# Kernel tuning notes

Hardware: AMD Instinct MI355X
Metric: run time of the kernel (lower is better)

## Reference

```python
import jax, jax.numpy as jnp
import numpy as np

TOP_K = 2
NUM_EXPERTS = 16
CAPACITY = 512          # >> avg load (128/expert) so no token is ever dropped in practice
FP8_MAX = 448.0         # float8_e4m3fn max representable magnitude


def _fp8_quant(v, axes):
    """Simulated fp8 e4m3 dynamic quantization: amax scaling + clipping.
    Returns (quantized values, scale with keepdims)."""
    s = jnp.clip(jnp.max(jnp.abs(v), axis=axes, keepdims=True) / FP8_MAX, 1e-12, None)
    return jnp.clip(v / s, -FP8_MAX, FP8_MAX), s


def setup_inputs() -> dict:
    key = jax.random.key(0)
    k0, k1, k2, k3 = jax.random.split(key, 4)
    T, H, I, E = 1024, 2048, 1408, NUM_EXPERTS
    x = jax.random.normal(k0, (T, H), jnp.float32)
    router_logits = jax.random.normal(k1, (T, E), jnp.float32)
    w13_weight = jax.random.normal(k2, (E, 2 * I, H), jnp.float32) * 0.02
    w2_weight = jax.random.normal(k3, (E, H, I), jnp.float32) * 0.02
    return {"x": x, "router_logits": router_logits,
            "w13_weight": w13_weight, "w2_weight": w2_weight}


def reference(x, router_logits, w13_weight, w2_weight):
    T, H = x.shape
    E, K, C = NUM_EXPERTS, TOP_K, CAPACITY
    I = w2_weight.shape[2]

    # --- routing: softmax -> top-k -> renormalize ---
    probs = jax.nn.softmax(router_logits, axis=-1)               # [T, E]
    topw, topi = jax.lax.top_k(probs, K)                          # [T, K]
    topw = topw / jnp.sum(topw, axis=-1, keepdims=True)

    # --- dispatch: flatten (token, k) rows, rank within expert ---
    rid = topi.reshape(-1)                                        # [T*K] expert id per row
    rtok = jnp.arange(T * K) // K                                 # source token per row
    order = jnp.argsort(rid)                                      # jax sort is stable
    counts = jnp.bincount(rid, length=E)
    offsets = jnp.concatenate([jnp.zeros(1, counts.dtype), jnp.cumsum(counts)[:-1]])
    pos_sorted = jnp.arange(T * K) - offsets[rid[order]]
    pos = jnp.zeros(T * K, jnp.int32).at[order].set(pos_sorted.astype(jnp.int32))
    valid = pos < C                                               # capacity is generous: no drops
    posc = jnp.minimum(pos, C - 1)

    xrows = x[rtok] * valid[:, None].astype(x.dtype)              # [T*K, H]
    xbuf = jnp.zeros((E, C, H), x.dtype).at[rid, posc].add(xrows)  # [E, C, H]

    # --- grouped GEMM 1 (gate+up), fp8 w8a8: per-expert weight scale, per-token act scale ---
    w13q, sw13 = _fp8_quant(w13_weight, (1, 2))                   # sw13 [E,1,1]
    xq, sa1 = _fp8_quant(xbuf, -1)                                # sa1  [E,C,1]
    h = jnp.einsum('ech,efh->ecf', xq, w13q) * (sa1 * sw13)       # [E, C, 2I]

    # --- silu_and_mul ---
    gate, up = h[..., :I], h[..., I:]
    act = jax.nn.silu(gate) * up                                  # [E, C, I]

    # --- grouped GEMM 2 (down) ---
    w2q, sw2 = _fp8_quant(w2_weight, (1, 2))                      # sw2 [E,1,1]
    aq, sa2 = _fp8_quant(act, -1)                                 # sa2 [E,C,1]
    ybuf = jnp.einsum('eci,ehi->ech', aq, w2q) * (sa2 * sw2)      # [E, C, H]

    # --- combine: gather back and weight by router probs ---
    yrows = ybuf[rid, posc] * valid[:, None].astype(x.dtype)      # [T*K, H]
    out = jnp.einsum('tkh,tk->th', yrows.reshape(T, K, H), topw)  # [T, H]
    return out
```

## Files before the change

kernel.cpp:

```cpp
#include <hip/hip_runtime.h>
#include <hip/hip_bf16.h>
#include <math.h>

#define NEXP 16
#define CAP  512
#define TTOK 1024
#define HDIM 2048
#define IDIM 1408

typedef float fx4 __attribute__((ext_vector_type(4)));
typedef short short8 __attribute__((ext_vector_type(8)));
typedef unsigned int u32;
typedef unsigned long long u64;

__device__ __forceinline__ unsigned short f2bf(float f) {
    u32 u = __float_as_uint(f);
    u += 0x7FFFu + ((u >> 16) & 1u);
    return (unsigned short)(u >> 16);
}
__device__ __forceinline__ float bf2f(unsigned short h) {
    return __uint_as_float(((u32)h) << 16);
}

__global__ void router_kernel(const float* __restrict__ logits,
                              int* __restrict__ topi, float* __restrict__ topw,
                              int* __restrict__ cnt1) {
    int t = blockIdx.x * blockDim.x + threadIdx.x;
    if (t >= TTOK) return;
    const float* l = logits + t * NEXP;
    float b0 = -INFINITY, b1 = -INFINITY; int i0 = 0, i1 = 0;
    for (int e = 0; e < NEXP; ++e) {
        float v = l[e];
        if (v > b0) { b1 = b0; i1 = i0; b0 = v; i0 = e; }
        else if (v > b1) { b1 = v; i1 = e; }
    }
    float w0 = 1.f / (1.f + expf(b1 - b0));
    topi[t*2]   = i0; topi[t*2+1] = i1;
    topw[t*2]   = w0; topw[t*2+1] = 1.f - w0;
    atomicAdd(&cnt1[i0], 1);
    atomicAdd(&cnt1[i1], 1);
}

__global__ void scan_kernel(const int* __restrict__ cnt1, int* __restrict__ base) {
    if (threadIdx.x == 0 && blockIdx.x == 0) {
        int s = 0;
        for (int e = 0; e < NEXP; ++e) {
            base[e] = s;
            int c = cnt1[e]; if (c > CAP) c = CAP;
            s += c;
        }
        base[NEXP] = s;
    }
}

__global__ void assign_kernel(const int* __restrict__ topi, const int* __restrict__ base,
                              int* __restrict__ cnt2,
                              int* __restrict__ slot_token, int* __restrict__ slot_of) {
    int t = blockIdx.x * blockDim.x + threadIdx.x;
    if (t >= TTOK) return;
    for (int k = 0; k < 2; ++k) {
        int e = topi[t*2+k];
        int p = atomicAdd(&cnt2[e], 1);
        if (p < CAP) {
            int s = base[e] + p;
            slot_token[s] = t;
            slot_of[t*2+k] = s;
        } else {
            slot_of[t*2+k] = -1;
        }
    }
}

#define LDA 40

template<int NDIM, int KDIM, bool GATHER>
__global__ __launch_bounds__(256) void gemm_bt_kernel(
    const float* __restrict__ Af32,
    const unsigned short* __restrict__ Abf16,
    const float* __restrict__ W,
    unsigned short* __restrict__ Cout,
    const int* __restrict__ slot_token,
    const int* __restrict__ base)
{
    const int e = blockIdx.z;
    const int n0 = base[e];
    const int rows = base[e+1] - n0;
    const int rtile = blockIdx.y * 128;
    if (rtile >= rows) return;
    const int col0 = blockIdx.x * 128;

    __shared__ unsigned short sA[128 * LDA];
    __shared__ unsigned short sB[128 * LDA];

    const int tid = threadIdx.x;
    const int lane = tid & 63;
    const int wv = tid >> 6;
    const int wm = wv >> 1, wn = wv & 1;
    const int lr = lane & 15;
    const int quad = lane >> 4;

    fx4 acc[4][4];
    #pragma unroll
    for (int i = 0; i < 4; ++i)
        #pragma unroll
        for (int j = 0; j < 4; ++j) acc[i][j] = (fx4)0.f;

    int tok[4];
    if (GATHER) {
        int rr = tid >> 3;
        #pragma unroll
        for (int p = 0; p < 4; ++p) {
            int grow = rtile + rr + p*32;
            tok[p] = (grow < rows) ? slot_token[n0 + grow] : -1;
        }
    } else {
        int rr = tid >> 2;
        #pragma unroll
        for (int p = 0; p < 2; ++p) {
            int grow = rtile + rr + p*64;
            tok[p] = (grow < rows) ? (n0 + grow) : -1;
        }
    }

    const float* Wp = W + ((size_t)e * NDIM + col0) * KDIM;

    const int KT = KDIM / 32;
    for (int kt = 0; kt < KT; ++kt) {
        const int k0 = kt * 32;
        __syncthreads();
        if (GATHER) {
            int g = tid & 7, rr = tid >> 3;
            #pragma unroll
            for (int p = 0; p < 4; ++p) {
                int row = rr + p*32;
                u64 v = 0;
                if (tok[p] >= 0) {
                    fx4 f = *(const fx4*)(Af32 + (size_t)tok[p]*KDIM + k0 + g*4);
                    u32 lo = (u32)f2bf(f.x) | ((u32)f2bf(f.y) << 16);
                    u32 hi = (u32)f2bf(f.z) | ((u32)f2bf(f.w) << 16);
                    v = (u64)lo | ((u64)hi << 32);
                }
                *(u64*)&sA[row*LDA + g*4] = v;
            }
        } else {
            int g = tid & 3, rr = tid >> 2;
            #pragma unroll
            for (int p = 0; p < 2; ++p) {
                int row = rr + p*64;
                fx4 v = (fx4)0.f;
                if (tok[p] >= 0)
                    v = *(const fx4*)(Abf16 + (size_t)tok[p]*KDIM + k0 + g*8);
                *(fx4*)&sA[row*LDA + g*8] = v;
            }
        }
        {
            int g = tid & 7, rr = tid >> 3;
            #pragma unroll
            for (int p = 0; p < 4; ++p) {
                int row = rr + p*32;
                fx4 f = *(const fx4*)(Wp + (size_t)row*KDIM + k0 + g*4);
                u32 lo = (u32)f2bf(f.x) | ((u32)f2bf(f.y) << 16);
                u32 hi = (u32)f2bf(f.z) | ((u32)f2bf(f.w) << 16);
                *(u64*)&sB[row*LDA + g*4] = (u64)lo | ((u64)hi << 32);
            }
        }
        __syncthreads();
        short8 af[4], bfr[4];
        #pragma unroll
        for (int mi = 0; mi < 4; ++mi) {
            int row = wm*64 + mi*16 + lr;
            af[mi] = *(const short8*)&sA[row*LDA + quad*8];
        }
        #pragma unroll
        for (int ni = 0; ni < 4; ++ni) {
            int row = wn*64 + ni*16 + lr;
            bfr[ni] = *(const short8*)&sB[row*LDA + quad*8];
        }
        #pragma unroll
        for (int mi = 0; mi < 4; ++mi)
            #pragma unroll
            for (int ni = 0; ni < 4; ++ni)
                acc[mi][ni] = __builtin_amdgcn_mfma_f32_16x16x32_bf16(
                    af[mi], bfr[ni], acc[mi][ni], 0, 0, 0);
    }

    #pragma unroll
    for (int mi = 0; mi < 4; ++mi) {
        #pragma unroll
        for (int r = 0; r < 4; ++r) {
            int grow = rtile + wm*64 + mi*16 + quad*4 + r;
            if (grow < rows) {
                size_t orow = (size_t)(n0 + grow) * NDIM;
                #pragma unroll
                for (int ni = 0; ni < 4; ++ni) {
                    int gcol = col0 + wn*64 + ni*16 + lr;
                    Cout[orow + gcol] = f2bf(acc[mi][ni][r]);
                }
            }
        }
    }
}

__global__ void silu_kernel(const unsigned short* __restrict__ h,
                            unsigned short* __restrict__ act,
                            const int* __restrict__ base) {
    const int R = base[NEXP];
    int idx = blockIdx.x * blockDim.x + threadIdx.x;
    int row = idx / (IDIM/8);
    int j   = idx % (IDIM/8);
    if (row >= R) return;
    const unsigned short* g = h + (size_t)row * (2*IDIM) + j*8;
    const unsigned short* u = g + IDIM;
    unsigned short go[8], uo[8], ao[8];
    *(fx4*)go = *(const fx4*)g;
    *(fx4*)uo = *(const fx4*)u;
    #pragma unroll
    for (int i = 0; i < 8; ++i) {
        float gv = bf2f(go[i]), uv = bf2f(uo[i]);
        float s = gv / (1.f + __expf(-gv));
        ao[i] = f2bf(s * uv);
    }
    *(fx4*)&act[(size_t)row*IDIM + j*8] = *(fx4*)ao;
}

__global__ void combine_kernel(const unsigned short* __restrict__ ybuf,
                               const int* __restrict__ slot_of,
                               const float* __restrict__ topw,
                               float* __restrict__ out) {
    int t = blockIdx.x;
    int c = threadIdx.x * 8;
    int s0 = slot_of[t*2], s1 = slot_of[t*2+1];
    float w0 = topw[t*2], w1 = topw[t*2+1];
    float res[8];
    #pragma unroll
    for (int i = 0; i < 8; ++i) res[i] = 0.f;
    if (s0 >= 0) {
        unsigned short y[8];
        *(fx4*)y = *(const fx4*)(ybuf + (size_t)s0*HDIM + c);
        #pragma unroll
        for (int i = 0; i < 8; ++i) res[i] += w0 * bf2f(y[i]);
    }
    if (s1 >= 0) {
        unsigned short y[8];
        *(fx4*)y = *(const fx4*)(ybuf + (size_t)s1*HDIM + c);
        #pragma unroll
        for (int i = 0; i < 8; ++i) res[i] += w1 * bf2f(y[i]);
    }
    float* o = out + (size_t)t*HDIM + c;
    *(fx4*)o       = *(fx4*)res;
    *(fx4*)(o + 4) = *(fx4*)(res + 4);
}

extern "C" void kernel_launch(void* const* d_in, const int* in_sizes, int n_in,
                              void* d_out, int out_size, void* d_ws, size_t ws_size,
                              hipStream_t stream) {
    const float* x      = (const float*)d_in[0];
    const float* logits = (const float*)d_in[1];
    const float* w13    = (const float*)d_in[2];
    const float* w2     = (const float*)d_in[3];
    float* out = (float*)d_out;

    char* ws = (char*)d_ws;
    size_t off = 0;
    auto alloc = [&](size_t bytes) -> void* {
        void* p = ws + off;
        off += (bytes + 255) & ~(size_t)255;
        return p;
    };
    int*   topi       = (int*)  alloc(TTOK*2*sizeof(int));
    float* topw       = (float*)alloc(TTOK*2*sizeof(float));
    int*   cnt1       = (int*)  alloc(NEXP*sizeof(int));
    int*   cnt2       = (int*)  alloc(NEXP*sizeof(int));
    int*   base       = (int*)  alloc((NEXP+1)*sizeof(int));
    int*   slot_token = (int*)  alloc(TTOK*2*sizeof(int));
    int*   slot_of    = (int*)  alloc(TTOK*2*sizeof(int));
    unsigned short* h    = (unsigned short*)alloc((size_t)TTOK*2 * (2*IDIM) * 2);
    unsigned short* act  = (unsigned short*)alloc((size_t)TTOK*2 * IDIM * 2);
    unsigned short* ybuf = (unsigned short*)alloc((size_t)TTOK*2 * HDIM * 2);

    hipMemsetAsync(cnt1, 0, NEXP*sizeof(int), stream);
    hipMemsetAsync(cnt2, 0, NEXP*sizeof(int), stream);

    router_kernel<<<dim3((TTOK+255)/256), 256, 0, stream>>>(logits, topi, topw, cnt1);
    scan_kernel<<<1, 64, 0, stream>>>(cnt1, base);
    assign_kernel<<<dim3((TTOK+255)/256), 256, 0, stream>>>(topi, base, cnt2, slot_token, slot_of);

    gemm_bt_kernel<2*IDIM, HDIM, true>
        <<<dim3(2*IDIM/128, CAP/128, NEXP), 256, 0, stream>>>(
            x, nullptr, w13, h, slot_token, base);

    silu_kernel<<<dim3((TTOK*2*(IDIM/8) + 255)/256), 256, 0, stream>>>(h, act, base);

    gemm_bt_kernel<HDIM, IDIM, false>
        <<<dim3(HDIM/128, CAP/128, NEXP), 256, 0, stream>>>(
            nullptr, act, w2, ybuf, slot_token, base);

    combine_kernel<<<dim3(TTOK), 256, 0, stream>>>(ybuf, slot_of, topw, out);
}
```

Before: 784.2 us.

## Double-buffer GEMM tiles with register prefetch and narrow N tile to 64

The grouped GEMM kernel now keeps two LDS buffers and loads the next K-slice's global data into registers while MFMAs run on the current slice, so there is one barrier per iteration instead of two. The output tile shrinks from 128x128 to 128x64, with each wave covering 32 rows by 64 columns, which doubles the grid along N. The goal is to hide global memory latency and raise the block count to fill the device. In exchange, A-tile loads and fp32-to-bf16 conversions are repeated across twice as many column blocks, and MFMA work per LDS load drops.

```diff
diff --git a/kernel.cpp b/kernel.cpp
--- a/kernel.cpp
+++ b/kernel.cpp
@@ -20,6 +20,11 @@
 }
 __device__ __forceinline__ float bf2f(unsigned short h) {
     return __uint_as_float(((u32)h) << 16);
+}
+__device__ __forceinline__ u64 pack4bf(fx4 f) {
+    u32 lo = (u32)f2bf(f.x) | ((u32)f2bf(f.y) << 16);
+    u32 hi = (u32)f2bf(f.z) | ((u32)f2bf(f.w) << 16);
+    return (u64)lo | ((u64)hi << 32);
 }
 
 __global__ void router_kernel(const float* __restrict__ logits,
@@ -87,113 +92,118 @@
     const int rows = base[e+1] - n0;
     const int rtile = blockIdx.y * 128;
     if (rtile >= rows) return;
-    const int col0 = blockIdx.x * 128;
-
-    __shared__ unsigned short sA[128 * LDA];
-    __shared__ unsigned short sB[128 * LDA];
+    const int col0 = blockIdx.x * 64;
+
+    __shared__ unsigned short sA[2][128 * LDA];
+    __shared__ unsigned short sB[2][64 * LDA];
 
     const int tid = threadIdx.x;
     const int lane = tid & 63;
     const int wv = tid >> 6;
-    const int wm = wv >> 1, wn = wv & 1;
     const int lr = lane & 15;
     const int quad = lane >> 4;
 
-    fx4 acc[4][4];
+    fx4 acc[2][4];
     #pragma unroll
-    for (int i = 0; i < 4; ++i)
+    for (int i = 0; i < 2; ++i)
         #pragma unroll
         for (int j = 0; j < 4; ++j) acc[i][j] = (fx4)0.f;
+
+    const int bg = tid & 7, bc = tid >> 3;
+    const int ag = tid & 7, ar = tid >> 3;
+    const int ag2 = tid & 3, ar2 = tid >> 2;
 
     int tok[4];
     if (GATHER) {
-        int rr = tid >> 3;
         #pragma unroll
         for (int p = 0; p < 4; ++p) {
-            int grow = rtile + rr + p*32;
+            int grow = rtile + ar + p*32;
             tok[p] = (grow < rows) ? slot_token[n0 + grow] : -1;
         }
     } else {
-        int rr = tid >> 2;
         #pragma unroll
         for (int p = 0; p < 2; ++p) {
-            int grow = rtile + rr + p*64;
+            int grow = rtile + ar2 + p*64;
             tok[p] = (grow < rows) ? (n0 + grow) : -1;
         }
     }
 
     const float* Wp = W + ((size_t)e * NDIM + col0) * KDIM;
+
+    fx4 pa[4], pb[2];
+
+    auto prefetch = [&](int k0) {
+        #pragma unroll
+        for (int p = 0; p < 2; ++p)
+            pb[p] = *(const fx4*)(Wp + (size_t)(bc + p*32) * KDIM + k0 + bg*4);
+        if (GATHER) {
+            #pragma unroll
+            for (int p = 0; p < 4; ++p)
+                pa[p] = (tok[p] >= 0)
+                    ? *(const fx4*)(Af32 + (size_t)tok[p]*KDIM + k0 + ag*4)
+                    : (fx4)0.f;
+        } else {
+            #pragma unroll
+            for (int p = 0; p < 2; ++p)
+                pa[p] = (tok[p] >= 0)
+                    ? *(const fx4*)(Abf16 + (size_t)tok[p]*KDIM + k0 + ag2*8)
+                    : (fx4)0.f;
+        }
+    };
+    auto stage = [&](int buf) {
+        #pragma unroll
+        for (int p = 0; p < 2; ++p)
+            *(u64*)&sB[buf][(bc + p*32)*LDA + bg*4] = pack4bf(pb[p]);
+        if (GATHER) {
+            #pragma unroll
+            for (int p = 0; p < 4; ++p)
+                *(u64*)&sA[buf][(ar + p*32)*LDA + ag*4] = pack4bf(pa[p]);
+        } else {
+            #pragma unroll
+            for (int p = 0; p < 2; ++p)
+                *(fx4*)&sA[buf][(ar2 + p*64)*LDA + ag2*8] = pa[p];
+        }
+    };
+
+    prefetch(0);
+    stage(0);
+    __syncthreads();
 
     const int KT = KDIM / 32;
     for (int kt = 0; kt < KT; ++kt) {
-        const int k0 = kt * 32;
-        __syncthreads();
-        if (GATHER) {
-            int g = tid & 7, rr = tid >> 3;
-            #pragma unroll
-            for (int p = 0; p < 4; ++p) {
-                int row = rr + p*32;
-                u64 v = 0;
-                if (tok[p] >= 0) {
-                    fx4 f = *(const fx4*)(Af32 + (size_t)tok[p]*KDIM + k0 + g*4);
-                    u32 lo = (u32)f2bf(f.x) | ((u32)f2bf(f.y) << 16);
-                    u32 hi = (u32)f2bf(f.z) | ((u32)f2bf(f.w) << 16);
-                    v = (u64)lo | ((u64)hi << 32);
-                }
-                *(u64*)&sA[row*LDA + g*4] = v;
-            }
-        } else {
-            int g = tid & 3, rr = tid >> 2;
-            #pragma unroll
-            for (int p = 0; p < 2; ++p) {
-                int row = rr + p*64;
-                fx4 v = (fx4)0.f;
-                if (tok[p] >= 0)
-                    v = *(const fx4*)(Abf16 + (size_t)tok[p]*KDIM + k0 + g*8);
-                *(fx4*)&sA[row*LDA + g*8] = v;
-            }
-        }
-        {
-            int g = tid & 7, rr = tid >> 3;
-            #pragma unroll
-            for (int p = 0; p < 4; ++p) {
-                int row = rr + p*32;
-                fx4 f = *(const fx4*)(Wp + (size_t)row*KDIM + k0 + g*4);
-                u32 lo = (u32)f2bf(f.x) | ((u32)f2bf(f.y) << 16);
-                u32 hi = (u32)f2bf(f.z) | ((u32)f2bf(f.w) << 16);
-                *(u64*)&sB[row*LDA + g*4] = (u64)lo | ((u64)hi << 32);
-            }
-        }
-        __syncthreads();
-        short8 af[4], bfr[4];
-        #pragma unroll
-        for (int mi = 0; mi < 4; ++mi) {
-            int row = wm*64 + mi*16 + lr;
-            af[mi] = *(const short8*)&sA[row*LDA + quad*8];
-        }
-        #pragma unroll
-        for (int ni = 0; ni < 4; ++ni) {
-            int row = wn*64 + ni*16 + lr;
-            bfr[ni] = *(const short8*)&sB[row*LDA + quad*8];
-        }
-        #pragma unroll
-        for (int mi = 0; mi < 4; ++mi)
+        const int cur = kt & 1;
+        if (kt + 1 < KT) prefetch((kt + 1) * 32);
+
+        short8 af[2], bfr[4];
+        #pragma unroll
+        for (int mi = 0; mi < 2; ++mi)
+            af[mi] = *(const short8*)&sA[cur][(wv*32 + mi*16 + lr)*LDA + quad*8];
+        #pragma unroll
+        for (int ni = 0; ni < 4; ++ni)
+            bfr[ni] = *(const short8*)&sB[cur][(ni*16 + lr)*LDA + quad*8];
+        #pragma unroll
+        for (int mi = 0; mi < 2; ++mi)
             #pragma unroll
             for (int ni = 0; ni < 4; ++ni)
                 acc[mi][ni] = __builtin_amdgcn_mfma_f32_16x16x32_bf16(
                     af[mi], bfr[ni], acc[mi][ni], 0, 0, 0);
+
+        if (kt + 1 < KT) {
+            stage(1 - cur);
+            __syncthreads();
+        }
     }
 
     #pragma unroll
-    for (int mi = 0; mi < 4; ++mi) {
+    for (int mi = 0; mi < 2; ++mi) {
         #pragma unroll
         for (int r = 0; r < 4; ++r) {
-            int grow = rtile + wm*64 + mi*16 + quad*4 + r;
+            int grow = rtile + wv*32 + mi*16 + quad*4 + r;
             if (grow < rows) {
                 size_t orow = (size_t)(n0 + grow) * NDIM;
                 #pragma unroll
                 for (int ni = 0; ni < 4; ++ni) {
-                    int gcol = col0 + wn*64 + ni*16 + lr;
+                    int gcol = col0 + ni*16 + lr;
                     Cout[orow + gcol] = f2bf(acc[mi][ni][r]);
                 }
             }
@@ -286,13 +296,13 @@
     assign_kernel<<<dim3((TTOK+255)/256), 256, 0, stream>>>(topi, base, cnt2, slot_token, slot_of);
 
     gemm_bt_kernel<2*IDIM, HDIM, true>
-        <<<dim3(2*IDIM/128, CAP/128, NEXP), 256, 0, stream>>>(
+        <<<dim3(2*IDIM/64, CAP/128, NEXP), 256, 0, stream>>>(
             x, nullptr, w13, h, slot_token, base);
 
     silu_kernel<<<dim3((TTOK*2*(IDIM/8) + 255)/256), 256, 0, stream>>>(h, act, base);
 
     gemm_bt_kernel<HDIM, IDIM, false>
-        <<<dim3(HDIM/128, CAP/128, NEXP), 256, 0, stream>>>(
+        <<<dim3(HDIM/64, CAP/128, NEXP), 256, 0, stream>>>(
             nullptr, act, w2, ybuf, slot_token, base);
 
     combine_kernel<<<dim3(TTOK), 256, 0, stream>>>(ybuf, slot_of, topw, out);
```

Result: faster. 758.5 us (-3.3%).
